# Performance work log

Hardware: AMD Instinct MI355X
Metric: run time of the kernel (lower is better)

The kernel has to match this reference:

```python
import jax, jax.numpy as jnp
import numpy as np

NUM_EMBEDDINGS = 1024
EMBEDDING_DIM = 256
COMMITMENT_COST = 0.25
B = 65536


def setup_inputs() -> dict:
    key = jax.random.key(0)
    k1, k2 = jax.random.split(key)
    inputs = jax.random.normal(k1, (B, EMBEDDING_DIM), dtype=jnp.float32)
    # torch init: uniform(-1/K, 1/K)
    W = jax.random.uniform(k2, (NUM_EMBEDDINGS, EMBEDDING_DIM), dtype=jnp.float32,
                           minval=-1.0 / NUM_EMBEDDINGS, maxval=1.0 / NUM_EMBEDDINGS)
    return {"inputs": inputs, "W": W}


def reference(inputs, W):
    x = inputs  # (B, D)
    # squared L2 distances to every codebook entry: (B, K)
    distances = (jnp.sum(x * x, axis=1, keepdims=True)
                 + jnp.sum(W * W, axis=1)
                 - 2.0 * jnp.matmul(x, W.T))
    idx = jnp.argmin(distances, axis=1)  # (B,)
    # one-hot @ W is just a gather
    quantized = jnp.take(W, idx, axis=0)  # (B, D)

    sg = jax.lax.stop_gradient
    e_latent_loss = jnp.mean((sg(quantized) - x) ** 2)
    q_latent_loss = jnp.mean((quantized - sg(x)) ** 2)
    loss = q_latent_loss + COMMITMENT_COST * e_latent_loss

    # perplexity from code-usage histogram (mean of one-hot rows)
    counts = jax.ops.segment_sum(jnp.ones((x.shape[0],), dtype=x.dtype), idx,
                                 num_segments=NUM_EMBEDDINGS)
    avg_probs = counts / x.shape[0]
    perplexity = jnp.exp(-jnp.sum(avg_probs * jnp.log(avg_probs + 1e-10)))

    # straight-through estimator
    quantized_st = x + sg(quantized - x)
    return quantized_st, loss, perplexity
```

## Files before the change

kernel.cpp:

```cpp
#include <hip/hip_runtime.h>


using h16   = _Float16;
using h16x8 = __attribute__((ext_vector_type(8))) _Float16;
using h16x4 = __attribute__((ext_vector_type(4))) _Float16;
using f32x4 = __attribute__((ext_vector_type(4))) float;

#define W_SCALE 1024.0f
#define W_UNSCALE2 0.001953125f
#define XS_STRIDE 264

__global__ __launch_bounds__(64) void vq_wconv(const float* __restrict__ W,
                                               h16* __restrict__ Whp,
                                               float* __restrict__ wws) {
  const int t = threadIdx.x;
  const int code = blockIdx.x * 2 + (t >> 5);
  const int j = t & 31;
  const int d0 = j * 8;
  float4 v0 = *(const float4*)(W + (size_t)code * 256 + d0);
  float4 v1 = *(const float4*)(W + (size_t)code * 256 + d0 + 4);
  h16x8 h;
  h[0] = (h16)(v0.x * W_SCALE); h[1] = (h16)(v0.y * W_SCALE);
  h[2] = (h16)(v0.z * W_SCALE); h[3] = (h16)(v0.w * W_SCALE);
  h[4] = (h16)(v1.x * W_SCALE); h[5] = (h16)(v1.y * W_SCALE);
  h[6] = (h16)(v1.z * W_SCALE); h[7] = (h16)(v1.w * W_SCALE);
  const int tile = code >> 4, ks = j >> 2, quad = j & 3, lm = code & 15;
  *(h16x8*)(Whp + (size_t)(((tile * 8 + ks) * 64 + quad * 16 + lm) * 8)) = h;
  float ss = v0.x * v0.x + v0.y * v0.y + v0.z * v0.z + v0.w * v0.w
           + v1.x * v1.x + v1.y * v1.y + v1.z * v1.z + v1.w * v1.w;
#pragma unroll
  for (int m = 1; m <= 16; m <<= 1) ss += __shfl_xor(ss, m);
  if (j == 0) wws[code] = ss;
}

__global__ __launch_bounds__(256, 2) void vq_main(const float* __restrict__ X,
                                                  const h16* __restrict__ Whp,
                                                  const float* __restrict__ wws,
                                                  const float* __restrict__ W,
                                                  float* __restrict__ out,
                                                  float* __restrict__ loss_sum,
                                                  int* __restrict__ counts) {
  __shared__ h16 Xs[128 * XS_STRIDE];
  __shared__ float redS[4 * 128];
  __shared__ int redC[4 * 128];
  __shared__ int sIdx[128];
  const int tid = threadIdx.x;
  const int lane = tid & 63;
  const int wid = tid >> 6;
  const int lm = lane & 15;
  const int quad = lane >> 4;
  const int rowBase = blockIdx.x * 128;

#pragma unroll
  for (int it = 0; it < 16; ++it) {
    int q = it * 256 + tid;
    int r = q >> 5;
    int dp = (q & 31) << 3;
    float4 v0 = *(const float4*)(X + (size_t)(rowBase + r) * 256 + dp);
    float4 v1 = *(const float4*)(X + (size_t)(rowBase + r) * 256 + dp + 4);
    h16x8 h;
    h[0] = (h16)v0.x; h[1] = (h16)v0.y; h[2] = (h16)v0.z; h[3] = (h16)v0.w;
    h[4] = (h16)v1.x; h[5] = (h16)v1.y; h[6] = (h16)v1.z; h[7] = (h16)v1.w;
    *(h16x8*)(Xs + r * XS_STRIDE + dp) = h;
  }
  __syncthreads();

  float bestS[32];
  int bestC[32];
#pragma unroll
  for (int s = 0; s < 32; ++s) { bestS[s] = 3.4e38f; bestC[s] = 0x7fffffff; }

  for (int chunk = 0; chunk < 8; ++chunk) {
    const int tbase = chunk * 8 + wid * 2;
    const h16* bptr = Whp + (size_t)(tbase * 8 * 64 + lane) * 8;
    f32x4 acc[8][2];
#pragma unroll
    for (int mt = 0; mt < 8; ++mt)
#pragma unroll
      for (int nt = 0; nt < 2; ++nt) {
        f32x4 z = {0.0f, 0.0f, 0.0f, 0.0f};
        acc[mt][nt] = z;
      }

#pragma unroll 2
    for (int ks = 0; ks < 8; ++ks) {
      h16x8 b0 = *(const h16x8*)(bptr + ks * 512);
      h16x8 b1 = *(const h16x8*)(bptr + ks * 512 + 4096);
      const int doff = ks * 32 + quad * 8;
#pragma unroll
      for (int mt = 0; mt < 8; ++mt) {
        h16x8 a = *(const h16x8*)(Xs + (mt * 16 + lm) * XS_STRIDE + doff);
        acc[mt][0] = __builtin_amdgcn_mfma_f32_16x16x32_f16(a, b0, acc[mt][0], 0, 0, 0);
        acc[mt][1] = __builtin_amdgcn_mfma_f32_16x16x32_f16(a, b1, acc[mt][1], 0, 0, 0);
      }
    }

#pragma unroll
    for (int nt = 0; nt < 2; ++nt) {
      int code = (tbase + nt) * 16 + lm;
      float wn = wws[code];
#pragma unroll
      for (int mt = 0; mt < 8; ++mt)
#pragma unroll
        for (int reg = 0; reg < 4; ++reg) {
          float s = fmaf(-W_UNSCALE2, acc[mt][nt][reg], wn);
          int slot = mt * 4 + reg;
          if (s < bestS[slot]) { bestS[slot] = s; bestC[slot] = code; }
        }
    }
  }

#pragma unroll
  for (int m = 1; m <= 8; m <<= 1) {
#pragma unroll
    for (int s = 0; s < 32; ++s) {
      float os = __shfl_xor(bestS[s], m);
      int oc = __shfl_xor(bestC[s], m);
      if (os < bestS[s] || (os == bestS[s] && oc < bestC[s])) { bestS[s] = os; bestC[s] = oc; }
    }
  }
  if (lm == 0) {
#pragma unroll
    for (int s = 0; s < 32; ++s) {
      int row = (s >> 2) * 16 + quad * 4 + (s & 3);
      redS[wid * 128 + row] = bestS[s];
      redC[wid * 128 + row] = bestC[s];
    }
  }
  __syncthreads();
  if (tid < 128) {
    float b = 3.4e38f;
    int c = 0x7fffffff;
#pragma unroll
    for (int w = 0; w < 4; ++w) {
      float s = redS[w * 128 + tid];
      int cc = redC[w * 128 + tid];
      if (s < b || (s == b && cc < c)) { b = s; c = cc; }
    }
    sIdx[tid] = c;
    atomicAdd(&counts[c], 1);
  }
  __syncthreads();

  float ll = 0.0f;
  const int d4 = lane << 2;
#pragma unroll 2
  for (int i = 0; i < 32; ++i) {
    int row = wid * 32 + i;
    int idx = sIdx[row];
    float4 qv = *(const float4*)(W + (size_t)idx * 256 + d4);
    h16x4 xh = *(const h16x4*)(Xs + row * XS_STRIDE + d4);
    float dx0 = qv.x - (float)xh[0];
    float dx1 = qv.y - (float)xh[1];
    float dx2 = qv.z - (float)xh[2];
    float dx3 = qv.w - (float)xh[3];
    ll += dx0 * dx0 + dx1 * dx1 + dx2 * dx2 + dx3 * dx3;
    *(float4*)(out + (size_t)(rowBase + row) * 256 + d4) = qv;
  }
#pragma unroll
  for (int m = 1; m <= 32; m <<= 1) ll += __shfl_xor(ll, m);
  if (lane == 0) atomicAdd(loss_sum, ll);
}

__global__ __launch_bounds__(256) void vq_finalize(const int* __restrict__ counts,
                                                   const float* __restrict__ loss_sum,
                                                   float* __restrict__ out) {
  __shared__ float red[256];
  const int tid = threadIdx.x;
  float h = 0.0f;
#pragma unroll
  for (int k = tid; k < 1024; k += 256) {
    float p = (float)counts[k] * (1.0f / 65536.0f);
    h += p * logf(p + 1e-10f);
  }
  red[tid] = h;
  __syncthreads();
#pragma unroll
  for (int s = 128; s > 0; s >>= 1) {
    if (tid < s) red[tid] += red[tid + s];
    __syncthreads();
  }
  if (tid == 0) {
    out[16777216] = loss_sum[0] * (1.25f / 16777216.0f);
    out[16777217] = expf(-red[0]);
  }
}

extern "C" void kernel_launch(void* const* d_in, const int* in_sizes, int n_in,
                              void* d_out, int out_size, void* d_ws, size_t ws_size,
                              hipStream_t stream) {
  (void)in_sizes; (void)n_in; (void)out_size; (void)ws_size;
  const float* X = (const float*)d_in[0];
  const float* W = (const float*)d_in[1];
  float* out = (float*)d_out;
  char* ws = (char*)d_ws;
  float* loss_sum = (float*)ws;
  int* counts = (int*)(ws + 256);
  float* wws = (float*)(ws + 4352);
  h16* Whp = (h16*)(ws + 8448);

  hipMemsetAsync(d_ws, 0, 4352, stream);
  vq_wconv<<<512, 64, 0, stream>>>(W, Whp, wws);
  vq_main<<<512, 256, 0, stream>>>(X, Whp, wws, W, out, loss_sum, counts);
  vq_finalize<<<1, 256, 0, stream>>>(counts, loss_sum, out);
}
```

Before: 189.1 us.

## Halve rows per block, compute loss from distances, use nontemporal loads/stores

Each block now handles 64 rows instead of 128, and the grid grows to 1024 blocks with launch bounds raised to 4 blocks per CU. The goal is better occupancy and more latency hiding while the MFMA work per wave is halved. The loss is now taken from the minimum distance plus the fp32 row norm computed during the X load, so the per-element difference loop over the gathered W rows is dropped. X loads and output stores use nontemporal hints. The trade-off is that W is reloaded from L2 twice as often, and the loss now depends on fp16-rounded dot products and may cancel numerically.

```diff
diff --git a/kernel.cpp b/kernel.cpp
--- a/kernel.cpp
+++ b/kernel.cpp
@@ -3,7 +3,6 @@
 
 using h16   = _Float16;
 using h16x8 = __attribute__((ext_vector_type(8))) _Float16;
-using h16x4 = __attribute__((ext_vector_type(4))) _Float16;
 using f32x4 = __attribute__((ext_vector_type(4))) float;
 
 #define W_SCALE 1024.0f
@@ -17,65 +16,74 @@
   const int code = blockIdx.x * 2 + (t >> 5);
   const int j = t & 31;
   const int d0 = j * 8;
-  float4 v0 = *(const float4*)(W + (size_t)code * 256 + d0);
-  float4 v1 = *(const float4*)(W + (size_t)code * 256 + d0 + 4);
+  f32x4 v0 = *(const f32x4*)(W + (size_t)code * 256 + d0);
+  f32x4 v1 = *(const f32x4*)(W + (size_t)code * 256 + d0 + 4);
   h16x8 h;
-  h[0] = (h16)(v0.x * W_SCALE); h[1] = (h16)(v0.y * W_SCALE);
-  h[2] = (h16)(v0.z * W_SCALE); h[3] = (h16)(v0.w * W_SCALE);
-  h[4] = (h16)(v1.x * W_SCALE); h[5] = (h16)(v1.y * W_SCALE);
-  h[6] = (h16)(v1.z * W_SCALE); h[7] = (h16)(v1.w * W_SCALE);
+  h[0] = (h16)(v0[0] * W_SCALE); h[1] = (h16)(v0[1] * W_SCALE);
+  h[2] = (h16)(v0[2] * W_SCALE); h[3] = (h16)(v0[3] * W_SCALE);
+  h[4] = (h16)(v1[0] * W_SCALE); h[5] = (h16)(v1[1] * W_SCALE);
+  h[6] = (h16)(v1[2] * W_SCALE); h[7] = (h16)(v1[3] * W_SCALE);
   const int tile = code >> 4, ks = j >> 2, quad = j & 3, lm = code & 15;
   *(h16x8*)(Whp + (size_t)(((tile * 8 + ks) * 64 + quad * 16 + lm) * 8)) = h;
-  float ss = v0.x * v0.x + v0.y * v0.y + v0.z * v0.z + v0.w * v0.w
-           + v1.x * v1.x + v1.y * v1.y + v1.z * v1.z + v1.w * v1.w;
+  float ss = v0[0] * v0[0] + v0[1] * v0[1] + v0[2] * v0[2] + v0[3] * v0[3]
+           + v1[0] * v1[0] + v1[1] * v1[1] + v1[2] * v1[2] + v1[3] * v1[3];
 #pragma unroll
   for (int m = 1; m <= 16; m <<= 1) ss += __shfl_xor(ss, m);
   if (j == 0) wws[code] = ss;
 }
 
-__global__ __launch_bounds__(256, 2) void vq_main(const float* __restrict__ X,
+__global__ __launch_bounds__(256, 4) void vq_main(const float* __restrict__ X,
                                                   const h16* __restrict__ Whp,
                                                   const float* __restrict__ wws,
                                                   const float* __restrict__ W,
                                                   float* __restrict__ out,
                                                   float* __restrict__ loss_sum,
                                                   int* __restrict__ counts) {
-  __shared__ h16 Xs[128 * XS_STRIDE];
-  __shared__ float redS[4 * 128];
-  __shared__ int redC[4 * 128];
-  __shared__ int sIdx[128];
+  __shared__ h16 Xs[64 * XS_STRIDE];
+  __shared__ float redS[4 * 64];
+  __shared__ int redC[4 * 64];
+  __shared__ int sIdx[64];
+  __shared__ float xnorm[64];
   const int tid = threadIdx.x;
   const int lane = tid & 63;
   const int wid = tid >> 6;
   const int lm = lane & 15;
   const int quad = lane >> 4;
-  const int rowBase = blockIdx.x * 128;
-
-#pragma unroll
-  for (int it = 0; it < 16; ++it) {
+  const int rowBase = blockIdx.x * 64;
+
+#pragma unroll
+  for (int it = 0; it < 8; ++it) {
     int q = it * 256 + tid;
     int r = q >> 5;
     int dp = (q & 31) << 3;
-    float4 v0 = *(const float4*)(X + (size_t)(rowBase + r) * 256 + dp);
-    float4 v1 = *(const float4*)(X + (size_t)(rowBase + r) * 256 + dp + 4);
+    const float* src = X + (size_t)(rowBase + r) * 256 + dp;
+    f32x4 v0 = __builtin_nontemporal_load((const f32x4*)src);
+    f32x4 v1 = __builtin_nontemporal_load((const f32x4*)src + 1);
     h16x8 h;
-    h[0] = (h16)v0.x; h[1] = (h16)v0.y; h[2] = (h16)v0.z; h[3] = (h16)v0.w;
-    h[4] = (h16)v1.x; h[5] = (h16)v1.y; h[6] = (h16)v1.z; h[7] = (h16)v1.w;
+    h[0] = (h16)v0[0]; h[1] = (h16)v0[1]; h[2] = (h16)v0[2]; h[3] = (h16)v0[3];
+    h[4] = (h16)v1[0]; h[5] = (h16)v1[1]; h[6] = (h16)v1[2]; h[7] = (h16)v1[3];
     *(h16x8*)(Xs + r * XS_STRIDE + dp) = h;
-  }
-  __syncthreads();
-
-  float bestS[32];
-  int bestC[32];
-#pragma unroll
-  for (int s = 0; s < 32; ++s) { bestS[s] = 3.4e38f; bestC[s] = 0x7fffffff; }
+    float ss = v0[0] * v0[0] + v0[1] * v0[1] + v0[2] * v0[2] + v0[3] * v0[3]
+             + v1[0] * v1[0] + v1[1] * v1[1] + v1[2] * v1[2] + v1[3] * v1[3];
+#pragma unroll
+    for (int m = 1; m <= 16; m <<= 1) ss += __shfl_xor(ss, m);
+    if ((q & 31) == 0) xnorm[r] = ss;
+  }
+  __syncthreads();
+
+  float bestS[16];
+  int bestC[16];
+#pragma unroll
+  for (int s = 0; s < 16; ++s) { bestS[s] = 3.4e38f; bestC[s] = 0x7fffffff; }
 
   for (int chunk = 0; chunk < 8; ++chunk) {
     const int tbase = chunk * 8 + wid * 2;
-    const h16* bptr = Whp + (size_t)(tbase * 8 * 64 + lane) * 8;
-    f32x4 acc[8][2];
-#pragma unroll
-    for (int mt = 0; mt < 8; ++mt)
+    const h16* bptr = Whp + (size_t)tbase * 4096 + lane * 8;
+    float wn0 = wws[tbase * 16 + lm];
+    float wn1 = wws[tbase * 16 + 16 + lm];
+    f32x4 acc[4][2];
+#pragma unroll
+    for (int mt = 0; mt < 4; ++mt)
 #pragma unroll
       for (int nt = 0; nt < 2; ++nt) {
         f32x4 z = {0.0f, 0.0f, 0.0f, 0.0f};
@@ -88,7 +96,7 @@
       h16x8 b1 = *(const h16x8*)(bptr + ks * 512 + 4096);
       const int doff = ks * 32 + quad * 8;
 #pragma unroll
-      for (int mt = 0; mt < 8; ++mt) {
+      for (int mt = 0; mt < 4; ++mt) {
         h16x8 a = *(const h16x8*)(Xs + (mt * 16 + lm) * XS_STRIDE + doff);
         acc[mt][0] = __builtin_amdgcn_mfma_f32_16x16x32_f16(a, b0, acc[mt][0], 0, 0, 0);
         acc[mt][1] = __builtin_amdgcn_mfma_f32_16x16x32_f16(a, b1, acc[mt][1], 0, 0, 0);
@@ -98,9 +106,9 @@
 #pragma unroll
     for (int nt = 0; nt < 2; ++nt) {
       int code = (tbase + nt) * 16 + lm;
-      float wn = wws[code];
-#pragma unroll
-      for (int mt = 0; mt < 8; ++mt)
+      float wn = nt ? wn1 : wn0;
+#pragma unroll
+      for (int mt = 0; mt < 4; ++mt)
 #pragma unroll
         for (int reg = 0; reg < 4; ++reg) {
           float s = fmaf(-W_UNSCALE2, acc[mt][nt][reg], wn);
@@ -113,7 +121,7 @@
 #pragma unroll
   for (int m = 1; m <= 8; m <<= 1) {
 #pragma unroll
-    for (int s = 0; s < 32; ++s) {
+    for (int s = 0; s < 16; ++s) {
       float os = __shfl_xor(bestS[s], m);
       int oc = __shfl_xor(bestC[s], m);
       if (os < bestS[s] || (os == bestS[s] && oc < bestC[s])) { bestS[s] = os; bestC[s] = oc; }
@@ -121,45 +129,39 @@
   }
   if (lm == 0) {
 #pragma unroll
-    for (int s = 0; s < 32; ++s) {
+    for (int s = 0; s < 16; ++s) {
       int row = (s >> 2) * 16 + quad * 4 + (s & 3);
-      redS[wid * 128 + row] = bestS[s];
-      redC[wid * 128 + row] = bestC[s];
-    }
-  }
-  __syncthreads();
-  if (tid < 128) {
+      redS[wid * 64 + row] = bestS[s];
+      redC[wid * 64 + row] = bestC[s];
+    }
+  }
+  __syncthreads();
+  if (wid == 0) {
     float b = 3.4e38f;
     int c = 0x7fffffff;
 #pragma unroll
     for (int w = 0; w < 4; ++w) {
-      float s = redS[w * 128 + tid];
-      int cc = redC[w * 128 + tid];
+      float s = redS[w * 64 + lane];
+      int cc = redC[w * 64 + lane];
       if (s < b || (s == b && cc < c)) { b = s; c = cc; }
     }
-    sIdx[tid] = c;
+    sIdx[lane] = c;
     atomicAdd(&counts[c], 1);
-  }
-  __syncthreads();
-
-  float ll = 0.0f;
+    float lossv = xnorm[lane] + b;
+#pragma unroll
+    for (int m = 1; m <= 32; m <<= 1) lossv += __shfl_xor(lossv, m);
+    if (lane == 0) atomicAdd(loss_sum, lossv);
+  }
+  __syncthreads();
+
   const int d4 = lane << 2;
 #pragma unroll 2
-  for (int i = 0; i < 32; ++i) {
-    int row = wid * 32 + i;
+  for (int i = 0; i < 16; ++i) {
+    int row = wid * 16 + i;
     int idx = sIdx[row];
-    float4 qv = *(const float4*)(W + (size_t)idx * 256 + d4);
-    h16x4 xh = *(const h16x4*)(Xs + row * XS_STRIDE + d4);
-    float dx0 = qv.x - (float)xh[0];
-    float dx1 = qv.y - (float)xh[1];
-    float dx2 = qv.z - (float)xh[2];
-    float dx3 = qv.w - (float)xh[3];
-    ll += dx0 * dx0 + dx1 * dx1 + dx2 * dx2 + dx3 * dx3;
-    *(float4*)(out + (size_t)(rowBase + row) * 256 + d4) = qv;
-  }
-#pragma unroll
-  for (int m = 1; m <= 32; m <<= 1) ll += __shfl_xor(ll, m);
-  if (lane == 0) atomicAdd(loss_sum, ll);
+    f32x4 qv = *(const f32x4*)(W + (size_t)idx * 256 + d4);
+    __builtin_nontemporal_store(qv, (f32x4*)(out + (size_t)(rowBase + row) * 256 + d4));
+  }
 }
 
 __global__ __launch_bounds__(256) void vq_finalize(const int* __restrict__ counts,
@@ -199,8 +201,8 @@
   float* wws = (float*)(ws + 4352);
   h16* Whp = (h16*)(ws + 8448);
 
-  hipMemsetAsync(d_ws, 0, 4352, stream);
+  (void)hipMemsetAsync(d_ws, 0, 4352, stream);
   vq_wconv<<<512, 64, 0, stream>>>(W, Whp, wws);
-  vq_main<<<512, 256, 0, stream>>>(X, Whp, wws, W, out, loss_sum, counts);
+  vq_main<<<1024, 256, 0, stream>>>(X, Whp, wws, W, out, loss_sum, counts);
   vq_finalize<<<1, 256, 0, stream>>>(counts, loss_sum, out);
 }
```

Result: faster. 179.4 us (-5.1%).
